# Optimization experiments

Hardware: AMD Instinct MI355X
Metric: run time of the kernel (lower is better)

## Reference

```python
import jax, jax.numpy as jnp
import numpy as np

# Coarse-to-fine lossless 3D segmentation (Seg3dLossless), batch=1, C=1.
RES = [17, 33, 65, 129]          # odd resolutions, stride (RF-1)/(R-1) is integral
RF = RES[-1]
B_MIN, B_MAX = -1.0, 1.0
BAL = 0.5                        # balance_value
N_CONFLICT_ITERS = 2             # fixed unroll of the data-dependent while-loop


def _mlp(pts, w1, b1, w2, b2, w3, b3):
    # query_func: occupancy MLP on normalized (x,y,z) points -> [N]
    h = jax.nn.relu(pts @ w1 + b1)
    h = jax.nn.relu(h @ w2 + b2)
    return jax.nn.sigmoid(h @ w3 + b3)[..., 0]


def _eval_grid(R, w1, b1, w2, b2, w3, b3):
    # batch_eval with align_corners=False: coords2D = (coord + 0.5)/RF, mapped to [B_MIN,B_MAX]
    s = (RF - 1) // (R - 1)
    c = jnp.arange(R, dtype=jnp.float32) * s                 # final-res integer coords
    p = (c + 0.5) / RF * (B_MAX - B_MIN) + B_MIN
    zz, yy, xx = jnp.meshgrid(p, p, p, indexing='ij')        # [D,H,W]
    pts = jnp.stack([xx, yy, zz], axis=-1).reshape(-1, 3)    # (x,y,z) order
    return _mlp(pts, w1, b1, w2, b2, w3, b3).reshape(R, R, R)


def _resize(x, R):
    # trilinear, align_corners=True: out index j -> in coord j*(in-1)/(out-1)
    c = jnp.linspace(0.0, x.shape[0] - 1.0, R)
    zz, yy, xx = jnp.meshgrid(c, c, c, indexing='ij')
    return jax.scipy.ndimage.map_coordinates(x, [zz, yy, xx], order=1, mode='nearest')


def _dilate(m):
    # smooth_conv3x3 (mean filter) followed by >0 == 3x3x3 binary dilation
    f = jax.lax.reduce_window(m.astype(jnp.float32), 0.0, jax.lax.max,
                              (3, 3, 3), (1, 1, 1), 'SAME')
    return f > 0.0


def setup_inputs() -> dict:
    key = jax.random.key(0)
    k1, k2, k3 = jax.random.split(key, 3)
    H = 64
    return {
        'w1': jax.random.normal(k1, (3, H), jnp.float32) * 0.8,
        'b1': jnp.zeros((H,), jnp.float32),
        'w2': jax.random.normal(k2, (H, H), jnp.float32) * (1.0 / np.sqrt(H)),
        'b2': jnp.zeros((H,), jnp.float32),
        'w3': jax.random.normal(k3, (H, 1), jnp.float32) * (1.0 / np.sqrt(H)),
        'b3': jnp.zeros((1,), jnp.float32),
    }


def reference(w1, b1, w2, b2, w3, b3):
    params = (w1, b1, w2, b2, w3, b3)
    # level 0: dense eval on the coarse grid
    occ = _eval_grid(RES[0], *params)                        # [R0,R0,R0]
    s0 = (RF - 1) // (RES[0] - 1)
    calculated = jnp.zeros((RF, RF, RF), bool).at[::s0, ::s0, ::s0].set(True)

    for R in RES[1:]:
        s = (RF - 1) // (R - 1)
        valid = _resize((occ > BAL).astype(jnp.float32), R)  # no-grad mask path
        occ_i = _resize(occ, R)                              # differentiable interp
        boundary = _dilate((valid > 0.0) & (valid < 1.0))
        calc_l = calculated[::s, ::s, ::s]
        boundary = boundary & (~calc_l)                      # skip already-evaluated voxels
        occ_true = _eval_grid(R, *params)                    # query_func at this level
        occ = jnp.where(boundary, occ_true, occ_i)           # scatter of occupancys_topk
        calc_l = calc_l | boundary
        # conflict resolution: re-query 3^3 neighbors of sign-flip voxels
        conflict = boundary & ((occ_i - BAL) * (occ_true - BAL) < 0.0)
        for _ in range(N_CONFLICT_ITERS):
            nbr = _dilate(conflict) & (~calc_l)
            occ_prev = occ
            occ = jnp.where(nbr, occ_true, occ)
            calc_l = calc_l | nbr
            conflict = nbr & ((occ_prev - BAL) * (occ_true - BAL) < 0.0)
        calculated = calculated.at[::s, ::s, ::s].set(calc_l)

    return occ[None, None]                                   # (1, 1, D, H, W)
```

## Files before the change

kernel.cpp:

```cpp
#include <hip/hip_runtime.h>

#define HH 64

static __global__ void k_set_ones(unsigned char* __restrict__ p, int n){
  int i = blockIdx.x * blockDim.x + threadIdx.x;
  if (i < n) p[i] = 1;
}

static __global__ void k_prep_w2t(const float* __restrict__ w2, float* __restrict__ w2t){
  int t = blockIdx.x * 256 + threadIdx.x;
  w2t[t] = w2[(t & 63) * HH + (t >> 6)];
}

__device__ __forceinline__ void mlp_pair(
    const float* __restrict__ sw1,
    const float* __restrict__ sw2t,
    const float* __restrict__ b2, const float* __restrict__ w3,
    const float* __restrict__ b3,
    float xA, float yA, float zA, float xB, float yB, float zB,
    float& outA, float& outB)
{
  const int ibase = ((threadIdx.x & 63) >> 5) * 32;
  float h1a[32], h1b[32];
  #pragma unroll
  for (int k = 0; k < 32; k += 4){
    const float4 wx = *(const float4*)&sw1[      ibase + k];
    const float4 wy = *(const float4*)&sw1[ 64 + ibase + k];
    const float4 wz = *(const float4*)&sw1[128 + ibase + k];
    const float4 bb = *(const float4*)&sw1[192 + ibase + k];
    h1a[k+0] = fmaxf(fmaf(xA,wx.x,fmaf(yA,wy.x,fmaf(zA,wz.x,bb.x))),0.f);
    h1a[k+1] = fmaxf(fmaf(xA,wx.y,fmaf(yA,wy.y,fmaf(zA,wz.y,bb.y))),0.f);
    h1a[k+2] = fmaxf(fmaf(xA,wx.z,fmaf(yA,wy.z,fmaf(zA,wz.z,bb.z))),0.f);
    h1a[k+3] = fmaxf(fmaf(xA,wx.w,fmaf(yA,wy.w,fmaf(zA,wz.w,bb.w))),0.f);
    h1b[k+0] = fmaxf(fmaf(xB,wx.x,fmaf(yB,wy.x,fmaf(zB,wz.x,bb.x))),0.f);
    h1b[k+1] = fmaxf(fmaf(xB,wx.y,fmaf(yB,wy.y,fmaf(zB,wz.y,bb.y))),0.f);
    h1b[k+2] = fmaxf(fmaf(xB,wx.z,fmaf(yB,wy.z,fmaf(zB,wz.z,bb.z))),0.f);
    h1b[k+3] = fmaxf(fmaf(xB,wx.w,fmaf(yB,wy.w,fmaf(zB,wz.w,bb.w))),0.f);
  }
  float oa = b3[0], ob = oa;
  #pragma unroll 1
  for (int j = 0; j < HH; ++j){
    const float4* wrow = (const float4*)&sw2t[j*HH + ibase];
    float a0 = 0.f, a1 = 0.f, c0 = 0.f, c1 = 0.f;
    #pragma unroll
    for (int q = 0; q < 8; q += 2){
      const float4 w0 = wrow[q];
      const float4 w1q = wrow[q+1];
      a0 = fmaf(h1a[4*q+0], w0.x, a0);
      a0 = fmaf(h1a[4*q+1], w0.y, a0);
      a0 = fmaf(h1a[4*q+2], w0.z, a0);
      a0 = fmaf(h1a[4*q+3], w0.w, a0);
      a1 = fmaf(h1a[4*q+4], w1q.x, a1);
      a1 = fmaf(h1a[4*q+5], w1q.y, a1);
      a1 = fmaf(h1a[4*q+6], w1q.z, a1);
      a1 = fmaf(h1a[4*q+7], w1q.w, a1);
      c0 = fmaf(h1b[4*q+0], w0.x, c0);
      c0 = fmaf(h1b[4*q+1], w0.y, c0);
      c0 = fmaf(h1b[4*q+2], w0.z, c0);
      c0 = fmaf(h1b[4*q+3], w0.w, c0);
      c1 = fmaf(h1b[4*q+4], w1q.x, c1);
      c1 = fmaf(h1b[4*q+5], w1q.y, c1);
      c1 = fmaf(h1b[4*q+6], w1q.z, c1);
      c1 = fmaf(h1b[4*q+7], w1q.w, c1);
    }
    float accA = a0 + a1, accB = c0 + c1;
    accA += __shfl_xor(accA, 32);
    accB += __shfl_xor(accB, 32);
    const float bj = b2[j], wj = w3[j];
    oa = fmaf(fmaxf(accA + bj, 0.f), wj, oa);
    ob = fmaf(fmaxf(accB + bj, 0.f), wj, ob);
  }
  outA = 1.f / (1.f + expf(-oa));
  outB = 1.f / (1.f + expf(-ob));
}

#define STAGE_WEIGHTS()                                            \
  __shared__ float sw1[4*HH];                                      \
  __shared__ float sw2t[HH*HH];                                    \
  {                                                                \
    const int t0 = threadIdx.x;                                    \
    if (t0 < 3*HH) sw1[t0] = w1[t0];                               \
    else sw1[t0] = b1[t0 - 3*HH];                                  \
    const float4* s4 = (const float4*)w2t;                         \
    float4* d4 = (float4*)sw2t;                                    \
    for (int i4 = t0; i4 < HH*HH/4; i4 += 256) d4[i4] = s4[i4];    \
    __syncthreads();                                               \
  }

static __global__ __launch_bounds__(256)
__attribute__((amdgpu_waves_per_eu(4,4)))
void k_eval_mlp(
    const float* __restrict__ w1, const float* __restrict__ b1,
    const float* __restrict__ w2t, const float* __restrict__ b2,
    const float* __restrict__ w3, const float* __restrict__ b3,
    float* __restrict__ out, int R, int s)
{
  STAGE_WEIGHTS();
  const unsigned int n = (unsigned int)R * (unsigned int)R * (unsigned int)R;
  const int lane = threadIdx.x & 63;
  const int wid = threadIdx.x >> 6;
  const unsigned int base = blockIdx.x * 256u + (unsigned int)(wid * 64 + (lane & 31));
  const unsigned int pidA = base < n ? base : (n - 1u);
  const unsigned int pB = base + 32u;
  const unsigned int pidB = pB < n ? pB : (n - 1u);
  const float inv129x2 = 2.0f / 129.0f;
  unsigned int cA = pidA % (unsigned int)R, rA = pidA / (unsigned int)R;
  unsigned int cB = pidB % (unsigned int)R, rB = pidB / (unsigned int)R;
  const float xA = ((float)(cA * (unsigned int)s) + 0.5f) * inv129x2 - 1.0f;
  const float yA = ((float)((rA % (unsigned int)R) * (unsigned int)s) + 0.5f) * inv129x2 - 1.0f;
  const float zA = ((float)((rA / (unsigned int)R) * (unsigned int)s) + 0.5f) * inv129x2 - 1.0f;
  const float xB = ((float)(cB * (unsigned int)s) + 0.5f) * inv129x2 - 1.0f;
  const float yB = ((float)((rB % (unsigned int)R) * (unsigned int)s) + 0.5f) * inv129x2 - 1.0f;
  const float zB = ((float)((rB / (unsigned int)R) * (unsigned int)s) + 0.5f) * inv129x2 - 1.0f;
  float oA, oB;
  mlp_pair(sw1, sw2t, b2, w3, b3, xA, yA, zA, xB, yB, zB, oA, oB);
  if ((threadIdx.x & 63) < 32){
    if (base < n) out[pidA] = oA;
    if (pB < n)   out[pidB] = oB;
  }
}

static __global__ __launch_bounds__(256)
__attribute__((amdgpu_waves_per_eu(4,4)))
void k_eval_sparse(
    const float* __restrict__ w1, const float* __restrict__ b1,
    const float* __restrict__ w2t, const float* __restrict__ b2,
    const float* __restrict__ w3, const float* __restrict__ b3,
    const int* __restrict__ idxl, const unsigned int* __restrict__ cnt,
    const float* __restrict__ occ_i,
    float* __restrict__ out, unsigned char* __restrict__ mism,
    int R, int s, unsigned int n)
{
  unsigned int count = *cnt;
  if (count > n) count = n;
  if (blockIdx.x * 256u >= count) return;
  STAGE_WEIGHTS();
  const int lane = threadIdx.x & 63;
  const int wid = threadIdx.x >> 6;
  const unsigned int slotA = blockIdx.x * 256u + (unsigned int)(wid * 64 + (lane & 31));
  const unsigned int slotB = slotA + 32u;
  const bool vA = slotA < count, vB = slotB < count;
  const unsigned int pidA = (unsigned int)idxl[vA ? slotA : 0];
  const unsigned int pidB = (unsigned int)idxl[vB ? slotB : 0];
  const float inv129x2 = 2.0f / 129.0f;
  unsigned int cA = pidA % (unsigned int)R, rA = pidA / (unsigned int)R;
  unsigned int cB = pidB % (unsigned int)R, rB = pidB / (unsigned int)R;
  const float xA = ((float)(cA * (unsigned int)s) + 0.5f) * inv129x2 - 1.0f;
  const float yA = ((float)((rA % (unsigned int)R) * (unsigned int)s) + 0.5f) * inv129x2 - 1.0f;
  const float zA = ((float)((rA / (unsigned int)R) * (unsigned int)s) + 0.5f) * inv129x2 - 1.0f;
  const float xB = ((float)(cB * (unsigned int)s) + 0.5f) * inv129x2 - 1.0f;
  const float yB = ((float)((rB % (unsigned int)R) * (unsigned int)s) + 0.5f) * inv129x2 - 1.0f;
  const float zB = ((float)((rB / (unsigned int)R) * (unsigned int)s) + 0.5f) * inv129x2 - 1.0f;
  float oA, oB;
  mlp_pair(sw1, sw2t, b2, w3, b3, xA, yA, zA, xB, yB, zB, oA, oB);
  if ((threadIdx.x & 63) < 32){
    if (vA){
      out[pidA] = oA;
      mism[pidA] = ((occ_i[pidA] - 0.5f) * (oA - 0.5f) < 0.0f) ? (unsigned char)1 : (unsigned char)0;
    }
    if (vB){
      out[pidB] = oB;
      mism[pidB] = ((occ_i[pidB] - 0.5f) * (oB - 0.5f) < 0.0f) ? (unsigned char)1 : (unsigned char)0;
    }
  }
}

static __global__ __launch_bounds__(256) void k_resize_b0(
    const float* __restrict__ prev,
    const unsigned char* __restrict__ calc_prev,
    float* __restrict__ occ_i, float* __restrict__ occ_out,
    unsigned char* __restrict__ bnd0, unsigned char* __restrict__ calc_out,
    unsigned char* __restrict__ confA, unsigned char* __restrict__ confB,
    unsigned char* __restrict__ upd, int R, int Rp)
{
  const unsigned int n = (unsigned int)R * (unsigned int)R * (unsigned int)R;
  unsigned int gid = blockIdx.x * 256u + threadIdx.x;
  if (gid >= n) return;
  int c = (int)(gid % (unsigned int)R);
  unsigned int r = gid / (unsigned int)R;
  int b = (int)(r % (unsigned int)R);
  int a = (int)(r / (unsigned int)R);
  int a0 = a >> 1, da = a & 1;
  int b0i = b >> 1, db = b & 1;
  int c0 = c >> 1, dc = c & 1;
  float sum = 0.0f;
  int cnt = 0;
  const int tot = (da + 1) * (db + 1) * (dc + 1);
  for (int dz = 0; dz <= da; ++dz)
    for (int dy = 0; dy <= db; ++dy)
      for (int dx = 0; dx <= dc; ++dx){
        float v = prev[((unsigned int)(a0 + dz) * (unsigned int)Rp + (unsigned int)(b0i + dy)) * (unsigned int)Rp + (unsigned int)(c0 + dx)];
        sum += v;
        cnt += (v > 0.5f) ? 1 : 0;
      }
  float oi = sum / (float)tot;
  occ_i[gid] = oi;
  occ_out[gid] = oi;
  bnd0[gid] = (cnt > 0 && cnt < tot) ? 1 : 0;
  calc_out[gid] = ((da | db | dc) == 0)
      ? calc_prev[((unsigned int)a0 * (unsigned int)Rp + (unsigned int)b0i) * (unsigned int)Rp + (unsigned int)c0]
      : (unsigned char)0;
  confA[gid] = 0; confB[gid] = 0; upd[gid] = 0;
}

static __global__ __launch_bounds__(256) void k_resize_boundary(
    const float* __restrict__ prev, const float* __restrict__ occ_true,
    const unsigned char* __restrict__ calc_prev,
    float* __restrict__ occ_i, float* __restrict__ occ_out,
    unsigned char* __restrict__ bnd0,
    unsigned char* __restrict__ mism, unsigned char* __restrict__ calc_out,
    int R, int Rp)
{
  const unsigned int n = (unsigned int)R * (unsigned int)R * (unsigned int)R;
  unsigned int gid = blockIdx.x * 256u + threadIdx.x;
  if (gid >= n) return;
  int c = (int)(gid % (unsigned int)R);
  unsigned int r = gid / (unsigned int)R;
  int b = (int)(r % (unsigned int)R);
  int a = (int)(r / (unsigned int)R);
  int a0 = a >> 1, da = a & 1;
  int b0i = b >> 1, db = b & 1;
  int c0 = c >> 1, dc = c & 1;
  float sum = 0.0f;
  int cnt = 0;
  const int tot = (da + 1) * (db + 1) * (dc + 1);
  for (int dz = 0; dz <= da; ++dz)
    for (int dy = 0; dy <= db; ++dy)
      for (int dx = 0; dx <= dc; ++dx){
        float v = prev[((unsigned int)(a0 + dz) * (unsigned int)Rp + (unsigned int)(b0i + dy)) * (unsigned int)Rp + (unsigned int)(c0 + dx)];
        sum += v;
        cnt += (v > 0.5f) ? 1 : 0;
      }
  float oi = sum / (float)tot;
  occ_i[gid] = oi;
  occ_out[gid] = oi;
  bnd0[gid] = (cnt > 0 && cnt < tot) ? 1 : 0;
  mism[gid] = ((oi - 0.5f) * (occ_true[gid] - 0.5f) < 0.0f) ? 1 : 0;
  calc_out[gid] = ((da | db | dc) == 0)
      ? calc_prev[((unsigned int)a0 * (unsigned int)Rp + (unsigned int)b0i) * (unsigned int)Rp + (unsigned int)c0]
      : (unsigned char)0;
}

static __global__ __launch_bounds__(256) void k_dil7x(
    const unsigned char* __restrict__ in, unsigned char* __restrict__ outp, int R)
{
  const unsigned int n = (unsigned int)R * (unsigned int)R * (unsigned int)R;
  unsigned int gid = blockIdx.x * 256u + threadIdx.x;
  if (gid >= n) return;
  int c = (int)(gid % (unsigned int)R);
  int g = (int)gid;
  int m = 0;
  #pragma unroll
  for (int d = -3; d <= 3; ++d){
    int q = c + d;
    if (q >= 0 && q < R) m |= in[g + d];
  }
  outp[gid] = (unsigned char)(m ? 1 : 0);
}

static __global__ __launch_bounds__(256) void k_dil7y(
    const unsigned char* __restrict__ in, unsigned char* __restrict__ outp, int R)
{
  const unsigned int n = (unsigned int)R * (unsigned int)R * (unsigned int)R;
  unsigned int gid = blockIdx.x * 256u + threadIdx.x;
  if (gid >= n) return;
  unsigned int r = gid / (unsigned int)R;
  int b = (int)(r % (unsigned int)R);
  int g = (int)gid;
  int m = 0;
  #pragma unroll
  for (int d = -3; d <= 3; ++d){
    int q = b + d;
    if (q >= 0 && q < R) m |= in[g + d * R];
  }
  outp[gid] = (unsigned char)(m ? 1 : 0);
}

static __global__ __launch_bounds__(256) void k_dil7z_count(
    const unsigned char* __restrict__ in, unsigned char* __restrict__ outp,
    unsigned int* __restrict__ bcnt, int R)
{
  const unsigned int n = (unsigned int)R * (unsigned int)R * (unsigned int)R;
  unsigned int gid = blockIdx.x * 256u + threadIdx.x;
  int m = 0;
  if (gid < n){
    int a = (int)(gid / ((unsigned int)R * (unsigned int)R));
    int g = (int)gid;
    int RR = R * R;
    #pragma unroll
    for (int d = -3; d <= 3; ++d){
      int q = a + d;
      if (q >= 0 && q < R) m |= in[g + d * RR];
    }
    outp[gid] = (unsigned char)(m ? 1 : 0);
  }
  unsigned long long bm = __ballot(m != 0);
  __shared__ unsigned int wc[4];
  int wid = (int)(threadIdx.x >> 6);
  if ((threadIdx.x & 63u) == 0) wc[wid] = (unsigned int)__popcll(bm);
  __syncthreads();
  if (threadIdx.x == 0) bcnt[blockIdx.x] = wc[0] + wc[1] + wc[2] + wc[3];
}

static __global__ __launch_bounds__(1024) void k_scan(
    unsigned int* __restrict__ bcnt, unsigned int nb, unsigned int* __restrict__ total)
{
  __shared__ unsigned int part[1024];
  const unsigned int t = threadIdx.x;
  const unsigned int chunk = (nb + 1023u) / 1024u;
  const unsigned int beg = t * chunk;
  const unsigned int end = (beg + chunk < nb) ? (beg + chunk) : nb;
  unsigned int s = 0;
  for (unsigned int i = beg; i < end; ++i) s += bcnt[i];
  part[t] = s;
  __syncthreads();
  for (int offd = 1; offd < 1024; offd <<= 1){
    unsigned int v = (t >= (unsigned int)offd) ? part[t - offd] : 0u;
    __syncthreads();
    part[t] += v;
    __syncthreads();
  }
  unsigned int run = (t == 0) ? 0u : part[t - 1];
  for (unsigned int i = beg; i < end; ++i){
    unsigned int v = bcnt[i];
    bcnt[i] = run;
    run += v;
  }
  if (t == 1023) *total = part[1023];
}

static __global__ __launch_bounds__(256) void k_scatter(
    const unsigned char* __restrict__ cand, const unsigned int* __restrict__ boff,
    int* __restrict__ idxl, unsigned int n)
{
  unsigned int gid = blockIdx.x * 256u + threadIdx.x;
  bool pred = (gid < n) && (cand[gid] != 0);
  unsigned long long m = __ballot(pred);
  __shared__ unsigned int wbase[4];
  int wid = (int)(threadIdx.x >> 6);
  int lane = (int)(threadIdx.x & 63u);
  if (lane == 0) wbase[wid] = (unsigned int)__popcll(m);
  __syncthreads();
  if (threadIdx.x == 0){
    unsigned int b = boff[blockIdx.x];
    unsigned int t0 = wbase[0], t1 = wbase[1], t2 = wbase[2];
    wbase[0] = b; wbase[1] = b + t0; wbase[2] = b + t0 + t1; wbase[3] = b + t0 + t1 + t2;
  }
  __syncthreads();
  if (pred){
    int pre = __popcll(m & ((1ull << lane) - 1ull));
    idxl[wbase[wid] + (unsigned int)pre] = (int)gid;
  }
}

static __global__ __launch_bounds__(256) void k_dilate_sparse(
    const int* __restrict__ idxl, const unsigned int* __restrict__ cnt,
    const unsigned char* __restrict__ src, const unsigned char* __restrict__ mism,
    unsigned char* __restrict__ calc, unsigned char* __restrict__ conf_out,
    unsigned char* __restrict__ upd, int R, int final_step,
    const float* __restrict__ occ_true, float* __restrict__ occ_out,
    unsigned int n)
{
  unsigned int count = *cnt;
  if (count > n) count = n;
  for (unsigned int slot = blockIdx.x * 256u + threadIdx.x; slot < count;
       slot += gridDim.x * 256u){
    int gid = idxl[slot];
    int c = gid % R;
    int r = gid / R;
    int b = r % R;
    int a = r / R;
    int m = 0;
    for (int dz = -1; dz <= 1; ++dz){
      int az = a + dz; if (az < 0 || az >= R) continue;
      for (int dy = -1; dy <= 1; ++dy){
        int by = b + dy; if (by < 0 || by >= R) continue;
        for (int dx = -1; dx <= 1; ++dx){
          int cx = c + dx; if (cx < 0 || cx >= R) continue;
          m |= src[(az * R + by) * R + cx];
        }
      }
    }
    unsigned char nb = (m && !calc[gid]) ? (unsigned char)1 : (unsigned char)0;
    conf_out[gid] = (nb && mism[gid]) ? (unsigned char)1 : (unsigned char)0;
    unsigned char u = upd[gid];
    if (nb){ calc[gid] = 1; if (!u){ upd[gid] = 1; u = 1; } }
    if (final_step && u) occ_out[gid] = occ_true[gid];
  }
}

static __global__ __launch_bounds__(256) void k_dilate_step(
    const unsigned char* __restrict__ src, const unsigned char* __restrict__ mism,
    unsigned char* __restrict__ calc, unsigned char* __restrict__ conf_out,
    unsigned char* __restrict__ upd, int R, int first, int final_step,
    const float* __restrict__ occ_true, float* __restrict__ occ_out)
{
  const unsigned int n = (unsigned int)R * (unsigned int)R * (unsigned int)R;
  unsigned int gid = blockIdx.x * 256u + threadIdx.x;
  if (gid >= n) return;
  int c = (int)(gid % (unsigned int)R);
  unsigned int r = gid / (unsigned int)R;
  int b = (int)(r % (unsigned int)R);
  int a = (int)(r / (unsigned int)R);
  int m = 0;
  for (int dz = -1; dz <= 1; ++dz){
    int az = a + dz; if (az < 0 || az >= R) continue;
    for (int dy = -1; dy <= 1; ++dy){
      int by = b + dy; if (by < 0 || by >= R) continue;
      for (int dx = -1; dx <= 1; ++dx){
        int cx = c + dx; if (cx < 0 || cx >= R) continue;
        m |= src[((unsigned int)az * (unsigned int)R + (unsigned int)by) * (unsigned int)R + (unsigned int)cx];
      }
    }
  }
  unsigned char nb = (m && !calc[gid]) ? (unsigned char)1 : (unsigned char)0;
  if (nb) calc[gid] = 1;
  conf_out[gid] = (nb && mism[gid]) ? (unsigned char)1 : (unsigned char)0;
  unsigned char u;
  if (first){ u = nb; upd[gid] = nb; }
  else { u = upd[gid]; if (nb && !u){ upd[gid] = 1; u = 1; } }
  if (final_step && u) occ_out[gid] = occ_true[gid];
}

extern "C" void kernel_launch(void* const* d_in, const int* in_sizes, int n_in,
                              void* d_out, int out_size, void* d_ws, size_t ws_size,
                              hipStream_t stream)
{
  const float* w1 = (const float*)d_in[0];
  const float* b1 = (const float*)d_in[1];
  const float* w2 = (const float*)d_in[2];
  const float* b2 = (const float*)d_in[3];
  const float* w3 = (const float*)d_in[4];
  const float* b3 = (const float*)d_in[5];
  float* out = (float*)d_out;

  const int NF = 129 * 129 * 129;
  const int NP = 65 * 65 * 65;
  char* ws = (char*)d_ws;
  size_t off = 0;
  auto alloc = [&](size_t bytes) -> void* {
    void* p = (void*)(ws + off);
    off += (bytes + 255) & ~(size_t)255;
    return p;
  };
  float* f_true  = (float*)alloc((size_t)NF * 4);
  float* f_occi  = (float*)alloc((size_t)NF * 4);
  float* f_prevA = (float*)alloc((size_t)NP * 4);
  float* f_prevB = (float*)alloc((size_t)NP * 4);
  float* f_w2t   = (float*)alloc((size_t)HH * HH * 4);
  int*   i_idx   = (int*)alloc((size_t)NF * 4);
  unsigned int* u_cnt  = (unsigned int*)alloc(256);
  unsigned int* u_bcnt = (unsigned int*)alloc(8448 * 4);
  unsigned char* b_b0    = (unsigned char*)alloc(NF);
  unsigned char* b_mism  = (unsigned char*)alloc(NF);
  unsigned char* b_confA = (unsigned char*)alloc(NF);
  unsigned char* b_confB = (unsigned char*)alloc(NF);
  unsigned char* b_calcA = (unsigned char*)alloc(NF);
  unsigned char* b_calcB = (unsigned char*)alloc(NF);
  unsigned char* b_upd   = (unsigned char*)alloc(NF);
  unsigned char* b_cand  = (unsigned char*)alloc(NF);
  unsigned char* b_tmp   = (unsigned char*)alloc(NF);
  (void)ws_size;

  k_prep_w2t<<<16, 256, 0, stream>>>(w2, f_w2t);

  {
    int R = 17, s = 8;
    int n = R * R * R;
    int blocks = (n + 255) / 256;
    k_eval_mlp<<<blocks, 256, 0, stream>>>(w1, b1, f_w2t, b2, w3, b3, f_prevA, R, s);
    k_set_ones<<<blocks, 256, 0, stream>>>(b_calcA, n);
  }

  int Rp = 17;
  float* prev = f_prevA;
  unsigned char* calcP = b_calcA;
  unsigned char* calcC = b_calcB;
  for (int li = 1; li <= 3; ++li){
    int R = 2 * Rp - 1;
    int s = 128 / (R - 1);
    unsigned int n = (unsigned int)R * (unsigned int)R * (unsigned int)R;
    int blocks = (int)((n + 255u) / 256u);
    float* occ_out = (li == 3) ? out : ((prev == f_prevA) ? f_prevB : f_prevA);

    if (R == 33){
      k_eval_mlp<<<blocks, 256, 0, stream>>>(w1, b1, f_w2t, b2, w3, b3, f_true, R, s);
      k_resize_boundary<<<blocks, 256, 0, stream>>>(prev, f_true, calcP, f_occi, occ_out, b_b0, b_mism, calcC, R, Rp);
      k_dilate_step<<<blocks, 256, 0, stream>>>(b_b0,    b_mism, calcC, b_confA, b_upd, R, 1, 0, f_true, occ_out);
      k_dilate_step<<<blocks, 256, 0, stream>>>(b_confA, b_mism, calcC, b_confB, b_upd, R, 0, 0, f_true, occ_out);
      k_dilate_step<<<blocks, 256, 0, stream>>>(b_confB, b_mism, calcC, b_confA, b_upd, R, 0, 1, f_true, occ_out);
    } else {
      k_resize_b0<<<blocks, 256, 0, stream>>>(prev, calcP, f_occi, occ_out, b_b0, calcC,
                                              b_confA, b_confB, b_upd, R, Rp);
      k_dil7x<<<blocks, 256, 0, stream>>>(b_b0,  b_tmp,  R);
      k_dil7y<<<blocks, 256, 0, stream>>>(b_tmp, b_cand, R);
      k_dil7z_count<<<blocks, 256, 0, stream>>>(b_cand, b_tmp, u_bcnt, R);
      k_scan<<<1, 1024, 0, stream>>>(u_bcnt, (unsigned int)blocks, u_cnt);
      k_scatter<<<blocks, 256, 0, stream>>>(b_tmp, u_bcnt, i_idx, n);
      k_eval_sparse<<<blocks, 256, 0, stream>>>(
          w1, b1, f_w2t, b2, w3, b3, i_idx, u_cnt, f_occi, f_true, b_mism, R, s, n);
      int sblocks = blocks < 4096 ? blocks : 4096;
      k_dilate_sparse<<<sblocks, 256, 0, stream>>>(i_idx, u_cnt, b_b0,    b_mism, calcC, b_confA, b_upd, R, 0, f_true, occ_out, n);
      k_dilate_sparse<<<sblocks, 256, 0, stream>>>(i_idx, u_cnt, b_confA, b_mism, calcC, b_confB, b_upd, R, 0, f_true, occ_out, n);
      k_dilate_sparse<<<sblocks, 256, 0, stream>>>(i_idx, u_cnt, b_confB, b_mism, calcC, b_confA, b_upd, R, 1, f_true, occ_out, n);
    }

    prev = occ_out;
    unsigned char* tmpc = calcP; calcP = calcC; calcC = tmpc;
    Rp = R;
  }
  (void)in_sizes; (void)n_in; (void)out_size;
}
```

Measured before the change: 308.0 us.

## Fuse 7x7x7 dilation into shared-memory tiles and evaluate R=65 level densely

The three separable 7-wide dilation passes for the sparse path become a single kernel that loads an 8^3 tile plus halo into shared memory and does the x, y and z passes there. The compaction scatter is rewritten to use the same tile ordering. The R=65 level switches from the sparse candidate list to a dense per-thread MLP evaluation that also computes the mismatch mask, followed by dense dilation steps. The set-ones kernel is folded into the first MLP eval. This removes global round trips and several launches, at the cost of dense MLP work on every R=65 voxel and a simpler, unshared-memory MLP kernel.

```diff
diff --git a/kernel.cpp b/kernel.cpp
--- a/kernel.cpp
+++ b/kernel.cpp
@@ -1,11 +1,6 @@
 #include <hip/hip_runtime.h>
 
 #define HH 64
-
-static __global__ void k_set_ones(unsigned char* __restrict__ p, int n){
-  int i = blockIdx.x * blockDim.x + threadIdx.x;
-  if (i < n) p[i] = 1;
-}
 
 static __global__ void k_prep_w2t(const float* __restrict__ w2, float* __restrict__ w2t){
   int t = blockIdx.x * 256 + threadIdx.x;
@@ -87,13 +82,41 @@
     __syncthreads();                                               \
   }
 
+__device__ __forceinline__ float mlp_eval_s(
+    const float* __restrict__ w1, const float* __restrict__ b1,
+    const float* __restrict__ w2t, const float* __restrict__ b2,
+    const float* __restrict__ w3, const float* __restrict__ b3,
+    float x, float y, float z)
+{
+  float h1[HH];
+  #pragma unroll
+  for (int i = 0; i < HH; ++i){
+    float v = b1[i];
+    v = fmaf(x, w1[i],        v);
+    v = fmaf(y, w1[HH + i],   v);
+    v = fmaf(z, w1[2*HH + i], v);
+    h1[i] = fmaxf(v, 0.0f);
+  }
+  float o = b3[0];
+  #pragma unroll 2
+  for (int j = 0; j < HH; ++j){
+    float acc = b2[j];
+    const float* wr = &w2t[j*HH];
+    #pragma unroll
+    for (int k = 0; k < HH; ++k) acc = fmaf(h1[k], wr[k], acc);
+    o = fmaf(fmaxf(acc, 0.0f), w3[j], o);
+  }
+  return 1.0f / (1.0f + expf(-o));
+}
+
 static __global__ __launch_bounds__(256)
 __attribute__((amdgpu_waves_per_eu(4,4)))
 void k_eval_mlp(
     const float* __restrict__ w1, const float* __restrict__ b1,
     const float* __restrict__ w2t, const float* __restrict__ b2,
     const float* __restrict__ w3, const float* __restrict__ b3,
-    float* __restrict__ out, int R, int s)
+    float* __restrict__ out, unsigned char* __restrict__ calc1,
+    int R, int s)
 {
   STAGE_WEIGHTS();
   const unsigned int n = (unsigned int)R * (unsigned int)R * (unsigned int)R;
@@ -115,9 +138,33 @@
   float oA, oB;
   mlp_pair(sw1, sw2t, b2, w3, b3, xA, yA, zA, xB, yB, zB, oA, oB);
   if ((threadIdx.x & 63) < 32){
-    if (base < n) out[pidA] = oA;
-    if (pB < n)   out[pidB] = oB;
-  }
+    if (base < n){ out[pidA] = oA; if (calc1) calc1[pidA] = 1; }
+    if (pB < n)  { out[pidB] = oB; if (calc1) calc1[pidB] = 1; }
+  }
+}
+
+static __global__ __launch_bounds__(256, 4) void k_eval_dense_mism(
+    const float* __restrict__ w1, const float* __restrict__ b1,
+    const float* __restrict__ w2t, const float* __restrict__ b2,
+    const float* __restrict__ w3, const float* __restrict__ b3,
+    const float* __restrict__ occ_i,
+    float* __restrict__ out, unsigned char* __restrict__ mism,
+    int R, int s)
+{
+  const unsigned int n = (unsigned int)R * (unsigned int)R * (unsigned int)R;
+  unsigned int pid = blockIdx.x * 256u + threadIdx.x;
+  if (pid >= n) return;
+  const unsigned int c = pid % (unsigned int)R;
+  const unsigned int r = pid / (unsigned int)R;
+  const unsigned int b = r % (unsigned int)R;
+  const unsigned int a = r / (unsigned int)R;
+  const float inv129x2 = 2.0f / 129.0f;
+  const float x = ((float)(c * (unsigned int)s) + 0.5f) * inv129x2 - 1.0f;
+  const float y = ((float)(b * (unsigned int)s) + 0.5f) * inv129x2 - 1.0f;
+  const float z = ((float)(a * (unsigned int)s) + 0.5f) * inv129x2 - 1.0f;
+  float ot = mlp_eval_s(w1, b1, w2t, b2, w3, b3, x, y, z);
+  out[pid] = ot;
+  mism[pid] = ((occ_i[pid] - 0.5f) * (ot - 0.5f) < 0.0f) ? (unsigned char)1 : (unsigned char)0;
 }
 
 static __global__ __launch_bounds__(256)
@@ -241,65 +288,53 @@
       : (unsigned char)0;
 }
 
-static __global__ __launch_bounds__(256) void k_dil7x(
-    const unsigned char* __restrict__ in, unsigned char* __restrict__ outp, int R)
-{
-  const unsigned int n = (unsigned int)R * (unsigned int)R * (unsigned int)R;
-  unsigned int gid = blockIdx.x * 256u + threadIdx.x;
-  if (gid >= n) return;
-  int c = (int)(gid % (unsigned int)R);
-  int g = (int)gid;
-  int m = 0;
-  #pragma unroll
-  for (int d = -3; d <= 3; ++d){
-    int q = c + d;
-    if (q >= 0 && q < R) m |= in[g + d];
-  }
-  outp[gid] = (unsigned char)(m ? 1 : 0);
-}
-
-static __global__ __launch_bounds__(256) void k_dil7y(
-    const unsigned char* __restrict__ in, unsigned char* __restrict__ outp, int R)
-{
-  const unsigned int n = (unsigned int)R * (unsigned int)R * (unsigned int)R;
-  unsigned int gid = blockIdx.x * 256u + threadIdx.x;
-  if (gid >= n) return;
-  unsigned int r = gid / (unsigned int)R;
-  int b = (int)(r % (unsigned int)R);
-  int g = (int)gid;
-  int m = 0;
-  #pragma unroll
-  for (int d = -3; d <= 3; ++d){
-    int q = b + d;
-    if (q >= 0 && q < R) m |= in[g + d * R];
-  }
-  outp[gid] = (unsigned char)(m ? 1 : 0);
-}
-
-static __global__ __launch_bounds__(256) void k_dil7z_count(
+static __global__ __launch_bounds__(512) void k_dil7_tiled(
     const unsigned char* __restrict__ in, unsigned char* __restrict__ outp,
-    unsigned int* __restrict__ bcnt, int R)
-{
-  const unsigned int n = (unsigned int)R * (unsigned int)R * (unsigned int)R;
-  unsigned int gid = blockIdx.x * 256u + threadIdx.x;
-  int m = 0;
-  if (gid < n){
-    int a = (int)(gid / ((unsigned int)R * (unsigned int)R));
-    int g = (int)gid;
-    int RR = R * R;
-    #pragma unroll
-    for (int d = -3; d <= 3; ++d){
-      int q = a + d;
-      if (q >= 0 && q < R) m |= in[g + d * RR];
-    }
-    outp[gid] = (unsigned char)(m ? 1 : 0);
-  }
-  unsigned long long bm = __ballot(m != 0);
-  __shared__ unsigned int wc[4];
-  int wid = (int)(threadIdx.x >> 6);
-  if ((threadIdx.x & 63u) == 0) wc[wid] = (unsigned int)__popcll(bm);
-  __syncthreads();
-  if (threadIdx.x == 0) bcnt[blockIdx.x] = wc[0] + wc[1] + wc[2] + wc[3];
+    unsigned int* __restrict__ bcnt, int R, int T)
+{
+  __shared__ unsigned char s0[14*14*14];
+  __shared__ unsigned char s1[14*14*8];
+  __shared__ unsigned char s2[14*8*8];
+  __shared__ unsigned int wc[8];
+  const int tile = blockIdx.x;
+  const int tz = tile / (T*T);
+  const int ty = (tile / T) % T;
+  const int tx = tile % T;
+  const int bz = tz*8 - 3, by = ty*8 - 3, bx = tx*8 - 3;
+  const int t = threadIdx.x;
+  for (int i = t; i < 14*14*14; i += 512){
+    int lz = i / 196, rr = i % 196, ly = rr / 14, lx = rr % 14;
+    int gz = bz + lz, gy = by + ly, gx = bx + lx;
+    unsigned char v = 0;
+    if (gz >= 0 && gz < R && gy >= 0 && gy < R && gx >= 0 && gx < R)
+      v = in[((unsigned int)gz * (unsigned int)R + (unsigned int)gy) * (unsigned int)R + (unsigned int)gx];
+    s0[i] = v;
+  }
+  __syncthreads();
+  for (int i = t; i < 14*14*8; i += 512){
+    int lz = i / 112, rr = i % 112, ly = rr / 8, lx = rr % 8;
+    const unsigned char* p = &s0[lz*196 + ly*14 + lx];
+    s1[i] = (unsigned char)(p[0]|p[1]|p[2]|p[3]|p[4]|p[5]|p[6]);
+  }
+  __syncthreads();
+  for (int i = t; i < 14*8*8; i += 512){
+    int lz = i / 64, rr = i % 64, ly = rr / 8, lx = rr % 8;
+    const unsigned char* p = &s1[lz*112 + ly*8 + lx];
+    s2[i] = (unsigned char)(p[0]|p[8]|p[16]|p[24]|p[32]|p[40]|p[48]);
+  }
+  __syncthreads();
+  int lz = t >> 6, ly = (t >> 3) & 7, lx = t & 7;
+  const unsigned char* p = &s2[lz*64 + ly*8 + lx];
+  int m = p[0]|p[64]|p[128]|p[192]|p[256]|p[320]|p[384];
+  int gz = tz*8 + lz, gy = ty*8 + ly, gx = tx*8 + lx;
+  bool inb = (gz < R) && (gy < R) && (gx < R);
+  if (inb) outp[((unsigned int)gz * (unsigned int)R + (unsigned int)gy) * (unsigned int)R + (unsigned int)gx]
+      = (unsigned char)(m ? 1 : 0);
+  unsigned long long bm = __ballot(inb && m);
+  int w = t >> 6;
+  if ((t & 63) == 0) wc[w] = (unsigned int)__popcll(bm);
+  __syncthreads();
+  if (t == 0) bcnt[blockIdx.x] = wc[0]+wc[1]+wc[2]+wc[3]+wc[4]+wc[5]+wc[6]+wc[7];
 }
 
 static __global__ __launch_bounds__(1024) void k_scan(
@@ -329,27 +364,31 @@
   if (t == 1023) *total = part[1023];
 }
 
-static __global__ __launch_bounds__(256) void k_scatter(
+static __global__ __launch_bounds__(512) void k_scatter_tiled(
     const unsigned char* __restrict__ cand, const unsigned int* __restrict__ boff,
-    int* __restrict__ idxl, unsigned int n)
-{
-  unsigned int gid = blockIdx.x * 256u + threadIdx.x;
-  bool pred = (gid < n) && (cand[gid] != 0);
+    int* __restrict__ idxl, int R, int T)
+{
+  __shared__ unsigned int wbase[8];
+  const int tile = blockIdx.x;
+  const int tz = tile / (T*T), ty = (tile / T) % T, tx = tile % T;
+  const int t = threadIdx.x;
+  int lz = t >> 6, ly = (t >> 3) & 7, lx = t & 7;
+  int gz = tz*8 + lz, gy = ty*8 + ly, gx = tx*8 + lx;
+  bool inb = (gz < R) && (gy < R) && (gx < R);
+  int gid = inb ? (int)(((unsigned int)gz * (unsigned int)R + (unsigned int)gy) * (unsigned int)R + (unsigned int)gx) : 0;
+  bool pred = inb && (cand[gid] != 0);
   unsigned long long m = __ballot(pred);
-  __shared__ unsigned int wbase[4];
-  int wid = (int)(threadIdx.x >> 6);
-  int lane = (int)(threadIdx.x & 63u);
-  if (lane == 0) wbase[wid] = (unsigned int)__popcll(m);
-  __syncthreads();
-  if (threadIdx.x == 0){
-    unsigned int b = boff[blockIdx.x];
-    unsigned int t0 = wbase[0], t1 = wbase[1], t2 = wbase[2];
-    wbase[0] = b; wbase[1] = b + t0; wbase[2] = b + t0 + t1; wbase[3] = b + t0 + t1 + t2;
+  int w = t >> 6, lane = t & 63;
+  if (lane == 0) wbase[w] = (unsigned int)__popcll(m);
+  __syncthreads();
+  if (t == 0){
+    unsigned int run = boff[blockIdx.x];
+    for (int i = 0; i < 8; ++i){ unsigned int v = wbase[i]; wbase[i] = run; run += v; }
   }
   __syncthreads();
   if (pred){
     int pre = __popcll(m & ((1ull << lane) - 1ull));
-    idxl[wbase[wid] + (unsigned int)pre] = (int)gid;
+    idxl[wbase[w] + (unsigned int)pre] = gid;
   }
 }
 
@@ -459,7 +498,6 @@
   unsigned char* b_calcB = (unsigned char*)alloc(NF);
   unsigned char* b_upd   = (unsigned char*)alloc(NF);
   unsigned char* b_cand  = (unsigned char*)alloc(NF);
-  unsigned char* b_tmp   = (unsigned char*)alloc(NF);
   (void)ws_size;
 
   k_prep_w2t<<<16, 256, 0, stream>>>(w2, f_w2t);
@@ -468,8 +506,7 @@
     int R = 17, s = 8;
     int n = R * R * R;
     int blocks = (n + 255) / 256;
-    k_eval_mlp<<<blocks, 256, 0, stream>>>(w1, b1, f_w2t, b2, w3, b3, f_prevA, R, s);
-    k_set_ones<<<blocks, 256, 0, stream>>>(b_calcA, n);
+    k_eval_mlp<<<blocks, 256, 0, stream>>>(w1, b1, f_w2t, b2, w3, b3, f_prevA, b_calcA, R, s);
   }
 
   int Rp = 17;
@@ -484,19 +521,26 @@
     float* occ_out = (li == 3) ? out : ((prev == f_prevA) ? f_prevB : f_prevA);
 
     if (R == 33){
-      k_eval_mlp<<<blocks, 256, 0, stream>>>(w1, b1, f_w2t, b2, w3, b3, f_true, R, s);
+      k_eval_mlp<<<blocks, 256, 0, stream>>>(w1, b1, f_w2t, b2, w3, b3, f_true, (unsigned char*)nullptr, R, s);
       k_resize_boundary<<<blocks, 256, 0, stream>>>(prev, f_true, calcP, f_occi, occ_out, b_b0, b_mism, calcC, R, Rp);
       k_dilate_step<<<blocks, 256, 0, stream>>>(b_b0,    b_mism, calcC, b_confA, b_upd, R, 1, 0, f_true, occ_out);
       k_dilate_step<<<blocks, 256, 0, stream>>>(b_confA, b_mism, calcC, b_confB, b_upd, R, 0, 0, f_true, occ_out);
       k_dilate_step<<<blocks, 256, 0, stream>>>(b_confB, b_mism, calcC, b_confA, b_upd, R, 0, 1, f_true, occ_out);
-    } else {
+    } else if (R == 65){
       k_resize_b0<<<blocks, 256, 0, stream>>>(prev, calcP, f_occi, occ_out, b_b0, calcC,
                                               b_confA, b_confB, b_upd, R, Rp);
-      k_dil7x<<<blocks, 256, 0, stream>>>(b_b0,  b_tmp,  R);
-      k_dil7y<<<blocks, 256, 0, stream>>>(b_tmp, b_cand, R);
-      k_dil7z_count<<<blocks, 256, 0, stream>>>(b_cand, b_tmp, u_bcnt, R);
-      k_scan<<<1, 1024, 0, stream>>>(u_bcnt, (unsigned int)blocks, u_cnt);
-      k_scatter<<<blocks, 256, 0, stream>>>(b_tmp, u_bcnt, i_idx, n);
+      k_eval_dense_mism<<<blocks, 256, 0, stream>>>(w1, b1, f_w2t, b2, w3, b3, f_occi, f_true, b_mism, R, s);
+      k_dilate_step<<<blocks, 256, 0, stream>>>(b_b0,    b_mism, calcC, b_confA, b_upd, R, 1, 0, f_true, occ_out);
+      k_dilate_step<<<blocks, 256, 0, stream>>>(b_confA, b_mism, calcC, b_confB, b_upd, R, 0, 0, f_true, occ_out);
+      k_dilate_step<<<blocks, 256, 0, stream>>>(b_confB, b_mism, calcC, b_confA, b_upd, R, 0, 1, f_true, occ_out);
+    } else {
+      const int T = (R + 7) / 8;
+      const int tblocks = T * T * T;
+      k_resize_b0<<<blocks, 256, 0, stream>>>(prev, calcP, f_occi, occ_out, b_b0, calcC,
+                                              b_confA, b_confB, b_upd, R, Rp);
+      k_dil7_tiled<<<tblocks, 512, 0, stream>>>(b_b0, b_cand, u_bcnt, R, T);
+      k_scan<<<1, 1024, 0, stream>>>(u_bcnt, (unsigned int)tblocks, u_cnt);
+      k_scatter_tiled<<<tblocks, 512, 0, stream>>>(b_cand, u_bcnt, i_idx, R, T);
       k_eval_sparse<<<blocks, 256, 0, stream>>>(
           w1, b1, f_w2t, b2, w3, b3, i_idx, u_cnt, f_occi, f_true, b_mism, R, s, n);
       int sblocks = blocks < 4096 ? blocks : 4096;
```

Result: slower. 321.4 us (+4.4%).
